# Performance work log

Measured on AMD Instinct MI355X. Metric: run time of the kernel, lower is better.

Reference implementation:

```python
import jax, jax.numpy as jnp
import numpy as np

B, T, D = 4, 4096, 4096
G, C, K, M = 1, 4, 128, 32          # num_groups, n_splits, dw_hidden_dim, heads_per_group
I2 = 4                               # qkw inner dim = 2 * dynamic_hidden_dim (dyn_hidden = 32//16 = 2)
EPS = 1.1920929e-07                  # torch F.rms_norm default eps for fp32


def _rms_norm(x):
    # F.rms_norm over last dim, no learned scale
    return x * jax.lax.rsqrt(jnp.mean(x * x, axis=-1, keepdims=True) + EPS)


def setup_inputs() -> dict:
    key = jax.random.key(0)
    k0, k1, k2, k3 = jax.random.split(key, 4)
    dw1_std = np.sqrt(2.0 / (D + K))
    qkw_std = 0.02 / (np.sqrt(2 * 32 * 2) * (32 + 2))
    dd_std = 0.05 * np.sqrt(2.0 / (32 + D))
    return {
        "query_vec": jax.random.normal(k0, (B, T, D), dtype=jnp.float32),
        "dw1": jax.random.normal(k1, (D, G, C, K), dtype=jnp.float32) * dw1_std,
        "qkw": jax.random.normal(k2, (G, C, K, I2, M), dtype=jnp.float32) * qkw_std,
        "dd": jax.random.normal(k3, (D, G, M * C), dtype=jnp.float32) * dd_std,
        "norm_scale": jnp.ones((G,), dtype=jnp.float32) * 0.001,
    }


def reference(query_vec, dw1, qkw, dd, norm_scale):
    # dw_hidden: [B,T,G,C,K]
    dw_hidden = jnp.einsum('btd,dgck->btgck', query_vec, dw1)
    dw_hidden = jax.nn.gelu(dw_hidden, approximate=False)  # torch nn.GELU() is exact
    # w: [B,T,G,C,I2,M]
    w = jnp.einsum('btgck,gckim->btgcim', dw_hidden, qkw)
    half = qkw.shape[-2] // 2
    w1 = _rms_norm(w[..., :half, :])
    w2 = _rms_norm(w[..., half:, :]) * norm_scale  # norm_scale [G]=(1,) broadcasts over M
    # squeeze group dim (keep_group_dim=False) -> [B,T,C,I,M]
    w1 = w1[:, :, 0]
    w2 = w2[:, :, 0]
    # unbind along C: order pre_q, pre_k, post_q, post_k; key-wise pieces are discarded
    pre_qw1, post_qw1 = w1[:, :, 0], w1[:, :, 2]
    pre_qw2, post_qw2 = w2[:, :, 0], w2[:, :, 2]
    # dd: [B,T,G,M*C] -> tanh -> squeeze G -> split 4
    dd_out = jnp.tanh(jnp.einsum('btd,dgm->btgm', query_vec, dd))[:, :, 0]
    pre_qdd = dd_out[..., 0 * M:1 * M]
    post_qdd = dd_out[..., 2 * M:3 * M]
    # pack all live outputs into one array [B, T, 2*(2*I*M) + 2*M]
    flat = lambda a: a.reshape(a.shape[0], a.shape[1], -1)
    return jnp.concatenate(
        [flat(pre_qw1), flat(pre_qw2), pre_qdd,
         flat(post_qw1), flat(post_qw2), post_qdd], axis=-1)
```

## Files before the change

kernel.cpp:

```cpp
#include <hip/hip_runtime.h>
#include <cstdint>
#include <cstddef>

typedef __bf16 bf16x8 __attribute__((ext_vector_type(8)));
typedef float f32x4 __attribute__((ext_vector_type(4)));

#define D_DIM 4096
#define NCOL 320
#define BM 64
#define NKT 128
#define EPS_F 1.1920929e-07f
#define HS 136
#define ABUF 8192
#define BBUF 20480
#define BUFS 28672

__device__ __forceinline__ void gld16(const void* g, void* l) {
  __builtin_amdgcn_global_load_lds(
      (const __attribute__((address_space(1))) unsigned int*)g,
      (__attribute__((address_space(3))) unsigned int*)l,
      16, 0, 0);
}

__global__ void dwp_pack(const float* __restrict__ dw1,
                         const float* __restrict__ qkw,
                         const float* __restrict__ dd,
                         __bf16* __restrict__ Wp,
                         __bf16* __restrict__ Qt) {
  const int tid = blockIdx.x * 256 + threadIdx.x;
  if (tid < 163840) {
    const int d = tid / 40;
    const int n = (tid % 40) * 8;
    const float* src;
    if (n < 128)       src = dw1 + (size_t)d * 512 + n;
    else if (n < 256)  src = dw1 + (size_t)d * 512 + 128 + n;
    else if (n < 288)  src = dd  + (size_t)d * 128 + (n - 256);
    else               src = dd  + (size_t)d * 128 + (n - 224);
    f32x4 v0 = *(const f32x4*)src;
    f32x4 v1 = *(const f32x4*)(src + 4);
    const int base = (d >> 5) * 10240 + n * 32 + (d & 31);
#pragma unroll
    for (int q = 0; q < 4; ++q) {
      Wp[base + q * 32] = (__bf16)v0[q];
      Wp[base + (q + 4) * 32] = (__bf16)v1[q];
    }
  } else if (tid < 167936) {
    const int q = tid - 163840;
    const int c2 = q >> 11;
    const int rem = q & 2047;
    const int n = rem >> 4;
    const int k0 = (rem & 15) * 8;
    const float* src = qkw + (size_t)c2 * 32768 + (size_t)k0 * 128 + n;
    bf16x8 v;
#pragma unroll
    for (int j = 0; j < 8; ++j) v[j] = (__bf16)src[(size_t)j * 128];
    *(bf16x8*)(Qt + (size_t)c2 * 16384 + (size_t)n * 128 + k0) = v;
  }
}

__global__ __launch_bounds__(512, 2) void dwp_main(
    const float* __restrict__ X,
    const __bf16* __restrict__ Wp,
    const __bf16* __restrict__ Qt,
    const float* __restrict__ NS,
    float* __restrict__ Out) {
  __shared__ __align__(16) unsigned char lds[2 * BUFS];
  const int t = threadIdx.x;
  const int w = t >> 6;
  const int l = t & 63;
  const int lq = l >> 4;
  const int lm = l & 15;
  const int m0 = blockIdx.x * BM;

  const float* gA = X + (size_t)(m0 + (t >> 3)) * D_DIM +
                    (size_t)(((t & 7) ^ ((t >> 3) & 7)) * 4);

  const int rbase = (w & 1) * 32;
  const int cbase = (w >> 1) * 80;

  unsigned aoff0[2], aoff1[2], boff[5];
#pragma unroll
  for (int rt = 0; rt < 2; ++rt) {
    const int row = rbase + rt * 16 + lm;
    aoff0[rt] = (unsigned)(row * 128 + (((lq * 2 + 0) ^ (lm & 7)) * 16));
    aoff1[rt] = (unsigned)(row * 128 + (((lq * 2 + 1) ^ (lm & 7)) * 16));
  }
#pragma unroll
  for (int ct = 0; ct < 5; ++ct)
    boff[ct] = (unsigned)(ABUF + ((cbase + ct * 16 + lm) * 32 + lq * 8) * 2);

  f32x4 acc[2][5];
#pragma unroll
  for (int rt = 0; rt < 2; ++rt)
#pragma unroll
    for (int ct = 0; ct < 5; ++ct)
      acc[rt][ct] = (f32x4){0.f, 0.f, 0.f, 0.f};

  auto issue = [&](int kt, int buf) {
    unsigned char* base = lds + buf * BUFS;
    const __bf16* wsrc = Wp + (size_t)kt * 10240;
    gld16(gA + (size_t)kt * 32, base + w * 1024);
    gld16(wsrc + (size_t)t * 8, base + ABUF + w * 1024);
    gld16(wsrc + (size_t)(4096 + t * 8), base + ABUF + 8192 + w * 1024);
    if (w < 4)
      gld16(wsrc + (size_t)(8192 + t * 8), base + ABUF + 16384 + w * 1024);
  };

  issue(0, 0);

  for (int kt = 0; kt < NKT; ++kt) {
    const int cur = kt & 1;
    __syncthreads();
    if (kt + 1 < NKT) issue(kt + 1, cur ^ 1);
    const unsigned char* cb = lds + cur * BUFS;
    bf16x8 a[2], b[5];
#pragma unroll
    for (int rt = 0; rt < 2; ++rt) {
      f32x4 x0 = *(const f32x4*)(cb + aoff0[rt]);
      f32x4 x1 = *(const f32x4*)(cb + aoff1[rt]);
#pragma unroll
      for (int j = 0; j < 4; ++j) {
        a[rt][j] = (__bf16)x0[j];
        a[rt][4 + j] = (__bf16)x1[j];
      }
    }
#pragma unroll
    for (int ct = 0; ct < 5; ++ct) b[ct] = *(const bf16x8*)(cb + boff[ct]);
#pragma unroll
    for (int rt = 0; rt < 2; ++rt)
#pragma unroll
      for (int ct = 0; ct < 5; ++ct)
        acc[rt][ct] =
            __builtin_amdgcn_mfma_f32_16x16x32_bf16(a[rt], b[ct], acc[rt][ct], 0, 0, 0);
  }

  __syncthreads();

  const float ns = NS[0];

#pragma unroll
  for (int rt = 0; rt < 2; ++rt) {
#pragma unroll
    for (int ct = 0; ct < 5; ++ct) {
      const int ncol = cbase + ct * 16 + lm;
      const int rowb = rbase + rt * 16 + lq * 4;
      f32x4 v = acc[rt][ct];
      if (ncol < 256) {
        const int c2 = ncol >> 7;
        const int kcol = ncol & 127;
#pragma unroll
        for (int j = 0; j < 4; ++j) {
          float x = v[j];
          float g = 0.5f * x * (1.0f + erff(x * 0.70710678118f));
          *(__bf16*)(lds + (size_t)((c2 * 64 + rowb + j) * HS + kcol) * 2) = (__bf16)g;
        }
      } else {
        const int nd = ncol - 256;
        const int off = (nd < 32) ? (128 + nd) : (256 + nd);
#pragma unroll
        for (int j = 0; j < 4; ++j)
          Out[(size_t)(m0 + rowb + j) * NCOL + off] = tanhf(v[j]);
      }
    }
  }
  __syncthreads();

  const int c2b = w >> 2;
  const int nnb = ((w >> 1) & 1) * 64;
  f32x4 acc2[2][4];
#pragma unroll
  for (int rt = 0; rt < 2; ++rt)
#pragma unroll
    for (int ct = 0; ct < 4; ++ct) acc2[rt][ct] = (f32x4){0.f, 0.f, 0.f, 0.f};

#pragma unroll
  for (int ks = 0; ks < 4; ++ks) {
    bf16x8 a2[2], b2[4];
#pragma unroll
    for (int rt = 0; rt < 2; ++rt)
      a2[rt] = *(const bf16x8*)(lds +
               (size_t)((c2b * 64 + rbase + rt * 16 + lm) * HS + ks * 32 + lq * 8) * 2);
#pragma unroll
    for (int ct = 0; ct < 4; ++ct)
      b2[ct] = *(const bf16x8*)(Qt + (size_t)c2b * 16384 +
               (size_t)(nnb + ct * 16 + lm) * 128 + ks * 32 + lq * 8);
#pragma unroll
    for (int rt = 0; rt < 2; ++rt)
#pragma unroll
      for (int ct = 0; ct < 4; ++ct)
        acc2[rt][ct] =
            __builtin_amdgcn_mfma_f32_16x16x32_bf16(a2[rt], b2[ct], acc2[rt][ct], 0, 0, 0);
  }

#pragma unroll
  for (int rt = 0; rt < 2; ++rt) {
#pragma unroll
    for (int p = 0; p < 2; ++p) {
      const int i = ((w >> 1) & 1) * 2 + p;
      const float sce = (i >= 2) ? ns : 1.0f;
      f32x4 va = acc2[rt][2 * p];
      f32x4 vb = acc2[rt][2 * p + 1];
#pragma unroll
      for (int j = 0; j < 4; ++j) {
        float s = va[j] * va[j] + vb[j] * vb[j];
        s += __shfl_xor(s, 1);
        s += __shfl_xor(s, 2);
        s += __shfl_xor(s, 4);
        s += __shfl_xor(s, 8);
        const float sc = rsqrtf(s * (1.0f / 32.0f) + EPS_F) * sce;
        const size_t row = (size_t)(m0 + rbase + rt * 16 + lq * 4 + j);
        const int off = c2b * 160 + i * 32;
        Out[row * NCOL + off + lm] = va[j] * sc;
        Out[row * NCOL + off + 16 + lm] = vb[j] * sc;
      }
    }
  }
}

extern "C" void kernel_launch(void* const* d_in, const int* in_sizes, int n_in,
                              void* d_out, int out_size, void* d_ws, size_t ws_size,
                              hipStream_t stream) {
  const float* qv  = (const float*)d_in[0];
  const float* dw1 = (const float*)d_in[1];
  const float* qkw = (const float*)d_in[2];
  const float* dd  = (const float*)d_in[3];
  const float* ns  = (const float*)d_in[4];
  float* out = (float*)d_out;

  __bf16* Wp = (__bf16*)d_ws;
  __bf16* Qt = Wp + (size_t)4096 * 320;

  dwp_pack<<<656, 256, 0, stream>>>(dw1, qkw, dd, Wp, Qt);
  dwp_main<<<256, 512, 0, stream>>>(qv, Wp, Qt, ns, out);
}
```

Measured before the change: 436.1 us.

## Deepen main GEMM pipeline to 4-stage LDS ring with explicit waitcnt barriers

```diff
diff --git a/kernel.cpp b/kernel.cpp
--- a/kernel.cpp
+++ b/kernel.cpp
@@ -11,9 +11,9 @@
 #define NKT 128
 #define EPS_F 1.1920929e-07f
 #define HS 136
-#define ABUF 8192
-#define BBUF 20480
-#define BUFS 28672
+#define STG 28672
+#define RING 4
+#define SMEM (RING * STG)
 
 __device__ __forceinline__ void gld16(const void* g, void* l) {
   __builtin_amdgcn_global_load_lds(
@@ -27,34 +27,52 @@
                          const float* __restrict__ dd,
                          __bf16* __restrict__ Wp,
                          __bf16* __restrict__ Qt) {
-  const int tid = blockIdx.x * 256 + threadIdx.x;
-  if (tid < 163840) {
-    const int d = tid / 40;
-    const int n = (tid % 40) * 8;
-    const float* src;
-    if (n < 128)       src = dw1 + (size_t)d * 512 + n;
-    else if (n < 256)  src = dw1 + (size_t)d * 512 + 128 + n;
-    else if (n < 288)  src = dd  + (size_t)d * 128 + (n - 256);
-    else               src = dd  + (size_t)d * 128 + (n - 224);
-    f32x4 v0 = *(const f32x4*)src;
-    f32x4 v1 = *(const f32x4*)(src + 4);
-    const int base = (d >> 5) * 10240 + n * 32 + (d & 31);
-#pragma unroll
-    for (int q = 0; q < 4; ++q) {
-      Wp[base + q * 32] = (__bf16)v0[q];
-      Wp[base + (q + 4) * 32] = (__bf16)v1[q];
-    }
-  } else if (tid < 167936) {
-    const int q = tid - 163840;
-    const int c2 = q >> 11;
-    const int rem = q & 2047;
-    const int n = rem >> 4;
-    const int k0 = (rem & 15) * 8;
-    const float* src = qkw + (size_t)c2 * 32768 + (size_t)k0 * 128 + n;
-    bf16x8 v;
-#pragma unroll
-    for (int j = 0; j < 8; ++j) v[j] = (__bf16)src[(size_t)j * 128];
-    *(bf16x8*)(Qt + (size_t)c2 * 16384 + (size_t)n * 128 + k0) = v;
+  const int b = blockIdx.x;
+  const int t = threadIdx.x;
+  if (b < 128) {
+    __shared__ __bf16 tile[10240];
+    const int kt = b;
+    const int kk = t >> 3;
+    const int d = kt * 32 + kk;
+    const int u = kk >> 3;
+#pragma unroll
+    for (int j = 0; j < 5; ++j) {
+      const int n0 = ((t & 7) + j * 8) * 8;
+      const float* src;
+      if (n0 < 128)      src = dw1 + (size_t)d * 512 + n0;
+      else if (n0 < 256) src = dw1 + (size_t)d * 512 + 128 + n0;
+      else if (n0 < 288) src = dd + (size_t)d * 128 + (n0 - 256);
+      else               src = dd + (size_t)d * 128 + (n0 - 224);
+      f32x4 v0 = *(const f32x4*)src;
+      f32x4 v1 = *(const f32x4*)(src + 4);
+#pragma unroll
+      for (int q = 0; q < 8; ++q) {
+        const int n = n0 + q;
+        const int pos = n * 32 + ((u ^ ((n >> 1) & 3)) << 3) + (kk & 7);
+        tile[pos] = (__bf16)((q < 4) ? v0[q] : v1[q - 4]);
+      }
+    }
+    __syncthreads();
+    __bf16* dst = Wp + (size_t)kt * 10240;
+#pragma unroll
+    for (int k = 0; k < 5; ++k) {
+      const int u16 = t + k * 256;
+      *(bf16x8*)(dst + u16 * 8) = *(const bf16x8*)(tile + u16 * 8);
+    }
+  } else {
+#pragma unroll
+    for (int ii = 0; ii < 16; ++ii) {
+      const int q = t + ii * 256;
+      const int c2 = q >> 11;
+      const int rem = q & 2047;
+      const int n = rem >> 4;
+      const int k0 = (rem & 15) * 8;
+      const float* src = qkw + (size_t)c2 * 32768 + (size_t)k0 * 128 + n;
+      bf16x8 v;
+#pragma unroll
+      for (int j = 0; j < 8; ++j) v[j] = (__bf16)src[(size_t)j * 128];
+      *(bf16x8*)(Qt + (size_t)c2 * 16384 + (size_t)n * 128 + k0) = v;
+    }
   }
 }
 
@@ -64,7 +82,7 @@
     const __bf16* __restrict__ Qt,
     const float* __restrict__ NS,
     float* __restrict__ Out) {
-  __shared__ __align__(16) unsigned char lds[2 * BUFS];
+  extern __shared__ __align__(16) unsigned char lds[];
   const int t = threadIdx.x;
   const int w = t >> 6;
   const int l = t & 63;
@@ -86,8 +104,10 @@
     aoff1[rt] = (unsigned)(row * 128 + (((lq * 2 + 1) ^ (lm & 7)) * 16));
   }
 #pragma unroll
-  for (int ct = 0; ct < 5; ++ct)
-    boff[ct] = (unsigned)(ABUF + ((cbase + ct * 16 + lm) * 32 + lq * 8) * 2);
+  for (int ct = 0; ct < 5; ++ct) {
+    const int n = cbase + ct * 16 + lm;
+    boff[ct] = (unsigned)(8192 + n * 64 + ((lq ^ ((n >> 1) & 3)) << 4));
+  }
 
   f32x4 acc[2][5];
 #pragma unroll
@@ -96,23 +116,18 @@
     for (int ct = 0; ct < 5; ++ct)
       acc[rt][ct] = (f32x4){0.f, 0.f, 0.f, 0.f};
 
-  auto issue = [&](int kt, int buf) {
-    unsigned char* base = lds + buf * BUFS;
+  auto issue = [&](int kt) {
+    unsigned char* base = lds + (kt & 3) * STG;
     const __bf16* wsrc = Wp + (size_t)kt * 10240;
     gld16(gA + (size_t)kt * 32, base + w * 1024);
-    gld16(wsrc + (size_t)t * 8, base + ABUF + w * 1024);
-    gld16(wsrc + (size_t)(4096 + t * 8), base + ABUF + 8192 + w * 1024);
+    gld16(wsrc + (size_t)t * 8, base + 8192 + w * 1024);
+    gld16(wsrc + (size_t)(4096 + t * 8), base + 16384 + w * 1024);
     if (w < 4)
-      gld16(wsrc + (size_t)(8192 + t * 8), base + ABUF + 16384 + w * 1024);
+      gld16(wsrc + (size_t)(8192 + t * 8), base + 24576 + w * 1024);
   };
 
-  issue(0, 0);
-
-  for (int kt = 0; kt < NKT; ++kt) {
-    const int cur = kt & 1;
-    __syncthreads();
-    if (kt + 1 < NKT) issue(kt + 1, cur ^ 1);
-    const unsigned char* cb = lds + cur * BUFS;
+  auto body = [&](int kt) {
+    const unsigned char* cb = lds + (kt & 3) * STG;
     bf16x8 a[2], b[5];
 #pragma unroll
     for (int rt = 0; rt < 2; ++rt) {
@@ -132,7 +147,26 @@
       for (int ct = 0; ct < 5; ++ct)
         acc[rt][ct] =
             __builtin_amdgcn_mfma_f32_16x16x32_bf16(a[rt], b[ct], acc[rt][ct], 0, 0, 0);
-  }
+  };
+
+  issue(0);
+  issue(1);
+  issue(2);
+
+  for (int kt = 0; kt < NKT - 2; ++kt) {
+    if (w < 4) asm volatile("s_waitcnt vmcnt(8) lgkmcnt(0)" ::: "memory");
+    else       asm volatile("s_waitcnt vmcnt(6) lgkmcnt(0)" ::: "memory");
+    asm volatile("s_barrier" ::: "memory");
+    if (kt + 3 < NKT) issue(kt + 3);
+    body(kt);
+  }
+  if (w < 4) asm volatile("s_waitcnt vmcnt(4) lgkmcnt(0)" ::: "memory");
+  else       asm volatile("s_waitcnt vmcnt(3) lgkmcnt(0)" ::: "memory");
+  asm volatile("s_barrier" ::: "memory");
+  body(NKT - 2);
+  asm volatile("s_waitcnt vmcnt(0) lgkmcnt(0)" ::: "memory");
+  asm volatile("s_barrier" ::: "memory");
+  body(NKT - 1);
 
   __syncthreads();
 
@@ -230,6 +264,9 @@
   __bf16* Wp = (__bf16*)d_ws;
   __bf16* Qt = Wp + (size_t)4096 * 320;
 
-  dwp_pack<<<656, 256, 0, stream>>>(dw1, qkw, dd, Wp, Qt);
-  dwp_main<<<256, 512, 0, stream>>>(qv, Wp, Qt, ns, out);
-}
+  hipFuncSetAttribute((const void*)dwp_main,
+                      hipFuncAttributeMaxDynamicSharedMemorySize, SMEM);
+
+  dwp_pack<<<129, 256, 0, stream>>>(dw1, qkw, dd, Wp, Qt);
+  dwp_main<<<256, 512, SMEM, stream>>>(qv, Wp, Qt, ns, out);
+}
```

After: 426.5 us. -2.2%, faster.
